# Optimization experiments

Hardware: AMD Instinct MI355X
Metric: run time of the kernel (lower is better)

Reference implementation:

```python
import jax, jax.numpy as jnp
import numpy as np

B, L, LO, H, V = 8, 1024, 1024, 768, 4096
NUM_TAGS = 256


def _merge_one(tags):
    """Replicates merge_weights() for one sequence of tags [L].

    A maximal run of equal, non-(-1) tags becomes one output row that averages
    the hidden states over the run. A run is only emitted when it is *closed*
    by a tag change or a -1 (so a run ending at the last position is dropped,
    exactly like the torch loop). Remaining rows are zero with bias -100.
    """
    Ls = tags.shape[0]
    pos = jnp.arange(Ls)
    valid = tags != -1
    prev = jnp.concatenate([jnp.full((1,), -2, tags.dtype), tags[:-1]])
    start = valid & ((pos == 0) | (tags != prev) | (prev == -1))
    seg_id = jnp.cumsum(start.astype(jnp.int32)) - 1          # run index per position
    total_runs = seg_id[-1] + 1
    emitted = total_runs - valid[-1].astype(jnp.int32)        # trailing open run dropped
    seg_clip = jnp.clip(seg_id, 0, Ls - 1)
    # run lengths via segment sum (invalid positions contribute 0)
    counts = jax.ops.segment_sum(valid.astype(jnp.float32), seg_clip, num_segments=Ls)
    w = jnp.where(valid & (seg_id >= 0) & (seg_id < emitted),
                  1.0 / jnp.maximum(counts[seg_clip], 1.0), 0.0)
    merge = jnp.zeros((Ls, Ls), jnp.float32).at[seg_clip, pos].add(w)  # [rows, tokens]
    bias = jnp.where(pos < emitted, 0.0, -100.0)
    return merge, bias


def setup_inputs() -> dict:
    key = jax.random.key(0)
    k1, k2, k3, k4 = jax.random.split(key, 4)
    hidden1_states = jax.random.normal(k1, (B, L, H), jnp.float32)
    hidden2_states = jax.random.normal(k2, (B, LO, H), jnp.float32)
    lm_logits = jax.random.normal(k3, (B, LO, V), jnp.float32)
    tags = jnp.sort(jax.random.randint(k4, (B, L), 0, NUM_TAGS), axis=-1)
    return {"hidden1_states": hidden1_states, "hidden2_states": hidden2_states,
            "lm_logits": lm_logits, "tags": tags}


def reference(hidden1_states, hidden2_states, lm_logits, tags):
    merge, bias = jax.vmap(_merge_one)(tags)                     # [B,L,L], [B,L]
    attn = jnp.einsum('bls,bsh->blh', merge, hidden1_states)     # segment means
    attn1 = jnp.einsum('boh,blh->bol', hidden2_states, attn) + bias[:, None, :]
    return jnp.concatenate([lm_logits, attn1], axis=2)           # [B,LO,V+L]
```

## Files before the change

### kernel.cpp

```cpp
#include <hip/hip_runtime.h>
#include <hip/hip_bf16.h>
#include <stdint.h>

#define BB   8
#define LL   1024
#define LOO  1024
#define HH   768
#define VV   4096
#define OUTW 5120
#define EMAX 256

typedef unsigned short ushort_t;
typedef __attribute__((ext_vector_type(4))) float   f32x4;
typedef __attribute__((ext_vector_type(8))) __bf16  bf16x8;
typedef __attribute__((ext_vector_type(4))) float   float4v;
typedef __attribute__((ext_vector_type(4))) int     int4v;

static __device__ __forceinline__ ushort_t f2bf(float f) {
    union { float f; uint32_t u; } v; v.f = f;
    uint32_t u = v.u;
    uint32_t r = (u + 0x7fffu + ((u >> 16) & 1u)) >> 16;
    return (ushort_t)r;
}

__global__ __launch_bounds__(256) void attn_fused_kernel(
        const float* __restrict__ h1,
        const int* __restrict__ tags,
        ushort_t* __restrict__ attn,
        int* __restrict__ emitted_out) {
    int b = blockIdx.x >> 8;
    int r = blockIdx.x & 255;
    int tid = threadIdx.x;

    __shared__ int stags[LL];
    __shared__ int cnt[256];
    __shared__ int runpos[EMAX + 2];

    ((int4v*)stags)[tid] = ((const int4v*)(tags + b * LL))[tid];
    __syncthreads();

    int p0 = tid * 4;
    int st[4];
    int prevm1 = (p0 == 0) ? -2 : stags[p0 - 1];
    st[0] = (p0 == 0) || (stags[p0] != prevm1);
    st[1] = (stags[p0 + 1] != stags[p0]);
    st[2] = (stags[p0 + 2] != stags[p0 + 1]);
    st[3] = (stags[p0 + 3] != stags[p0 + 2]);
    int c = st[0] + st[1] + st[2] + st[3];
    cnt[tid] = c;
    __syncthreads();
    for (int off = 1; off < 256; off <<= 1) {
        int v = cnt[tid];
        int a = (tid >= off) ? cnt[tid - off] : 0;
        __syncthreads();
        cnt[tid] = v + a;
        __syncthreads();
    }
    int total = cnt[255];
    int base = cnt[tid] - c;
#pragma unroll
    for (int j = 0; j < 4; ++j)
        if (st[j]) runpos[base++] = p0 + j;
    if (tid == 0) runpos[total] = LL;
    __syncthreads();

    int em = total - 1;
    if (r == 0 && tid == 0) emitted_out[b] = em;

    ushort_t* arow = attn + ((size_t)b * EMAX + r) * HH;
    if (r >= em) {
        arow[tid] = 0; arow[tid + 256] = 0; arow[tid + 512] = 0;
        return;
    }
    int s = runpos[r], e = runpos[r + 1];
    float inv = 1.0f / (float)(e - s);
    const float* hb = h1 + (size_t)b * LL * HH;
    float a0 = 0.f, a1 = 0.f, a2 = 0.f;
    for (int p = s; p < e; ++p) {
        const float* row = hb + (size_t)p * HH;
        a0 += row[tid]; a1 += row[tid + 256]; a2 += row[tid + 512];
    }
    arow[tid]       = f2bf(a0 * inv);
    arow[tid + 256] = f2bf(a1 * inv);
    arow[tid + 512] = f2bf(a2 * inv);
}

#define NGEMM 128
#define NCOPY 2048
__global__ __launch_bounds__(256, 2) void mega_kernel(
        const float* __restrict__ A,
        const ushort_t* __restrict__ Bm,
        const int* __restrict__ emitted,
        const float* __restrict__ lm,
        float* __restrict__ out) {
    __shared__ char smem[49152];

    if (blockIdx.x >= NGEMM) {
        int cid = blockIdx.x - NGEMM;
        int tid = threadIdx.x;
        const float4v* in4 = (const float4v*)lm;
        float4v* out4 = (float4v*)out;
        int c = cid * 256 + tid;
#pragma unroll
        for (int g = 0; g < 4; ++g) {
            size_t i0 = (size_t)(g * 4 + 0) * 524288 + c;
            size_t i1 = (size_t)(g * 4 + 1) * 524288 + c;
            size_t i2 = (size_t)(g * 4 + 2) * 524288 + c;
            size_t i3 = (size_t)(g * 4 + 3) * 524288 + c;
            float4v v0 = in4[i0];
            float4v v1 = in4[i1];
            float4v v2 = in4[i2];
            float4v v3 = in4[i3];
            out4[i0 + ((i0 >> 10) << 8)] = v0;
            out4[i1 + ((i1 >> 10) << 8)] = v1;
            out4[i2 + ((i2 >> 10) << 8)] = v2;
            out4[i3 + ((i3 >> 10) << 8)] = v3;
        }
        float4v fv = {-100.f, -100.f, -100.f, -100.f};
        if (tid < 192) {
#pragma unroll
            for (int j = 0; j < 4; ++j) {
                size_t row = (size_t)cid * 4 + j;
                out4[row * (OUTW / 4) + (VV + 256) / 4 + tid] = fv;
            }
        }
        return;
    }

    int bid  = blockIdx.x;
    int b    = bid >> 4;
    int t2   = bid & 15;
    int brow = (t2 >> 1) << 7;
    int bcol = (t2 & 1) << 7;

    const int tid  = threadIdx.x;
    const int lane = tid & 63;
    const int wid  = tid >> 6;
    const int wr   = (wid >> 1) & 1;
    const int wc   = wid & 1;

    const float*    Ab = A  + (size_t)b * LOO * HH;
    const ushort_t* Bb = Bm + (size_t)b * EMAX * HH;

    f32x4 zero = {0.f, 0.f, 0.f, 0.f};
    f32x4 acc[4][4];
#pragma unroll
    for (int i = 0; i < 4; ++i)
#pragma unroll
        for (int j = 0; j < 4; ++j) acc[i][j] = zero;

    for (int k0 = 0; k0 < HH; k0 += 64) {
        __syncthreads();
#pragma unroll
        for (int i = 0; i < 8; ++i) {
            int off = i * 4096 + tid * 16;
            int row = off >> 8;
            int cb  = off & 255;
            int scb = cb ^ ((row & 7) << 5);
            const float* ga = Ab + (size_t)(brow + row) * HH + k0 + (scb >> 2);
            __builtin_amdgcn_global_load_lds(
                (const __attribute__((address_space(1))) void*)ga,
                (__attribute__((address_space(3))) void*)(smem + off), 16, 0, 0);
        }
#pragma unroll
        for (int i = 0; i < 4; ++i) {
            int off = i * 4096 + tid * 16;
            int row = off >> 7;
            int cb  = off & 127;
            int scb = cb ^ ((row & 7) << 4);
            const ushort_t* gb = Bb + (size_t)(bcol + row) * HH + k0 + (scb >> 1);
            __builtin_amdgcn_global_load_lds(
                (const __attribute__((address_space(1))) void*)gb,
                (__attribute__((address_space(3))) void*)(smem + 32768 + off), 16, 0, 0);
        }
        asm volatile("s_waitcnt vmcnt(0)" ::: "memory");
        __syncthreads();

#pragma unroll
        for (int ks = 0; ks < 2; ++ks) {
            bf16x8 af[4], bfr[4];
#pragma unroll
            for (int mi = 0; mi < 4; ++mi) {
                int row  = (wr << 6) + (mi << 4) + (lane & 15);
                int colb = (ks << 7) + ((lane >> 4) << 5);
                int addr = (row << 8) + (colb ^ ((row & 7) << 5));
                f32x4 a0 = *(const f32x4*)(smem + addr);
                f32x4 a1 = *(const f32x4*)(smem + addr + 16);
                bf16x8 t;
                t[0] = (__bf16)a0[0]; t[1] = (__bf16)a0[1];
                t[2] = (__bf16)a0[2]; t[3] = (__bf16)a0[3];
                t[4] = (__bf16)a1[0]; t[5] = (__bf16)a1[1];
                t[6] = (__bf16)a1[2]; t[7] = (__bf16)a1[3];
                af[mi] = t;
            }
#pragma unroll
            for (int ni = 0; ni < 4; ++ni) {
                int row  = (wc << 6) + (ni << 4) + (lane & 15);
                int colb = (ks << 6) + ((lane >> 4) << 4);
                int addr = (row << 7) + (colb ^ ((row & 7) << 4));
                bfr[ni] = *(const bf16x8*)(smem + 32768 + addr);
            }
#pragma unroll
            for (int mi = 0; mi < 4; ++mi)
#pragma unroll
                for (int ni = 0; ni < 4; ++ni)
                    acc[mi][ni] = __builtin_amdgcn_mfma_f32_16x16x32_bf16(
                        af[mi], bfr[ni], acc[mi][ni], 0, 0, 0);
        }
    }

    int em = emitted[b];
    float* outb = out + (size_t)b * LOO * OUTW + VV;
#pragma unroll
    for (int mi = 0; mi < 4; ++mi) {
        int rbase = brow + (wr << 6) + (mi << 4) + ((lane >> 4) << 2);
#pragma unroll
        for (int ni = 0; ni < 4; ++ni) {
            int col = bcol + (wc << 6) + (ni << 4) + (lane & 15);
            float badd = (col < em) ? 0.0f : -100.0f;
#pragma unroll
            for (int rr = 0; rr < 4; ++rr)
                outb[(size_t)(rbase + rr) * OUTW + col] = acc[mi][ni][rr] + badd;
        }
    }
}

extern "C" void kernel_launch(void* const* d_in, const int* in_sizes, int n_in,
                              void* d_out, int out_size, void* d_ws, size_t ws_size,
                              hipStream_t stream) {
    const float* h1   = (const float*)d_in[0];
    const float* h2   = (const float*)d_in[1];
    const float* lm   = (const float*)d_in[2];
    const int*   tags = (const int*)d_in[3];
    float* out = (float*)d_out;

    char* ws = (char*)d_ws;
    ushort_t* attn    = (ushort_t*)ws;
    int*      emitted = (int*)(ws + 3145728);

    attn_fused_kernel<<<BB * EMAX, 256, 0, stream>>>(h1, tags, attn, emitted);
    mega_kernel<<<NGEMM + NCOPY, 256, 0, stream>>>(h2, attn, emitted, lm, out);
}
```

Measured before the change: 85.08 us.

## Drop LDS staging in GEMM and use smaller 128x64 tiles with more blocks

The GEMM portion no longer stages A and B tiles through shared memory with global_load_lds. Each wave now loads its MFMA fragments straight from global memory, converting fp32 to bf16 in registers. The output tile shrinks from 128x128 to 128x64, which doubles the GEMM block count to 256 and raises the occupancy hint to 4 blocks per SM. The aim is to remove LDS round trips and barriers and to spread the GEMM over more CUs alongside the copy blocks. The cost is that operands are re-read from global or cache by several waves, and the fragment loads are less coalesced.

```diff
diff --git a/kernel.cpp b/kernel.cpp
--- a/kernel.cpp
+++ b/kernel.cpp
@@ -85,15 +85,14 @@
     arow[tid + 512] = f2bf(a2 * inv);
 }
 
-#define NGEMM 128
+#define NGEMM 256
 #define NCOPY 2048
-__global__ __launch_bounds__(256, 2) void mega_kernel(
+__global__ __launch_bounds__(256, 4) void mega_kernel(
         const float* __restrict__ A,
         const ushort_t* __restrict__ Bm,
         const int* __restrict__ emitted,
         const float* __restrict__ lm,
         float* __restrict__ out) {
-    __shared__ char smem[49152];
 
     if (blockIdx.x >= NGEMM) {
         int cid = blockIdx.x - NGEMM;
@@ -128,10 +127,10 @@
     }
 
     int bid  = blockIdx.x;
-    int b    = bid >> 4;
-    int t2   = bid & 15;
-    int brow = (t2 >> 1) << 7;
-    int bcol = (t2 & 1) << 7;
+    int b    = bid >> 5;
+    int t2   = bid & 31;
+    int brow = (t2 >> 2) << 7;
+    int bcol = (t2 & 3) << 6;
 
     const int tid  = threadIdx.x;
     const int lane = tid & 63;
@@ -142,71 +141,39 @@
     const float*    Ab = A  + (size_t)b * LOO * HH;
     const ushort_t* Bb = Bm + (size_t)b * EMAX * HH;
 
+    const int arow0 = brow + (wr << 6) + (lane & 15);
+    const int brow0 = bcol + (wc << 5) + (lane & 15);
+    const int ksub  = (lane >> 4) << 3;
+
     f32x4 zero = {0.f, 0.f, 0.f, 0.f};
-    f32x4 acc[4][4];
-#pragma unroll
-    for (int i = 0; i < 4; ++i)
-#pragma unroll
-        for (int j = 0; j < 4; ++j) acc[i][j] = zero;
-
-    for (int k0 = 0; k0 < HH; k0 += 64) {
-        __syncthreads();
-#pragma unroll
-        for (int i = 0; i < 8; ++i) {
-            int off = i * 4096 + tid * 16;
-            int row = off >> 8;
-            int cb  = off & 255;
-            int scb = cb ^ ((row & 7) << 5);
-            const float* ga = Ab + (size_t)(brow + row) * HH + k0 + (scb >> 2);
-            __builtin_amdgcn_global_load_lds(
-                (const __attribute__((address_space(1))) void*)ga,
-                (__attribute__((address_space(3))) void*)(smem + off), 16, 0, 0);
-        }
-#pragma unroll
-        for (int i = 0; i < 4; ++i) {
-            int off = i * 4096 + tid * 16;
-            int row = off >> 7;
-            int cb  = off & 127;
-            int scb = cb ^ ((row & 7) << 4);
-            const ushort_t* gb = Bb + (size_t)(bcol + row) * HH + k0 + (scb >> 1);
-            __builtin_amdgcn_global_load_lds(
-                (const __attribute__((address_space(1))) void*)gb,
-                (__attribute__((address_space(3))) void*)(smem + 32768 + off), 16, 0, 0);
-        }
-        asm volatile("s_waitcnt vmcnt(0)" ::: "memory");
-        __syncthreads();
-
-#pragma unroll
-        for (int ks = 0; ks < 2; ++ks) {
-            bf16x8 af[4], bfr[4];
-#pragma unroll
-            for (int mi = 0; mi < 4; ++mi) {
-                int row  = (wr << 6) + (mi << 4) + (lane & 15);
-                int colb = (ks << 7) + ((lane >> 4) << 5);
-                int addr = (row << 8) + (colb ^ ((row & 7) << 5));
-                f32x4 a0 = *(const f32x4*)(smem + addr);
-                f32x4 a1 = *(const f32x4*)(smem + addr + 16);
-                bf16x8 t;
-                t[0] = (__bf16)a0[0]; t[1] = (__bf16)a0[1];
-                t[2] = (__bf16)a0[2]; t[3] = (__bf16)a0[3];
-                t[4] = (__bf16)a1[0]; t[5] = (__bf16)a1[1];
-                t[6] = (__bf16)a1[2]; t[7] = (__bf16)a1[3];
-                af[mi] = t;
-            }
-#pragma unroll
-            for (int ni = 0; ni < 4; ++ni) {
-                int row  = (wc << 6) + (ni << 4) + (lane & 15);
-                int colb = (ks << 6) + ((lane >> 4) << 4);
-                int addr = (row << 7) + (colb ^ ((row & 7) << 4));
-                bfr[ni] = *(const bf16x8*)(smem + 32768 + addr);
-            }
-#pragma unroll
-            for (int mi = 0; mi < 4; ++mi)
-#pragma unroll
-                for (int ni = 0; ni < 4; ++ni)
-                    acc[mi][ni] = __builtin_amdgcn_mfma_f32_16x16x32_bf16(
-                        af[mi], bfr[ni], acc[mi][ni], 0, 0, 0);
-        }
+    f32x4 acc[4][2];
+#pragma unroll
+    for (int i = 0; i < 4; ++i) { acc[i][0] = zero; acc[i][1] = zero; }
+
+#pragma unroll 2
+    for (int k0 = 0; k0 < HH; k0 += 32) {
+        bf16x8 af[4], bfr[2];
+#pragma unroll
+        for (int mi = 0; mi < 4; ++mi) {
+            const float* pa = Ab + (size_t)(arow0 + (mi << 4)) * HH + k0 + ksub;
+            f32x4 a0 = *(const f32x4*)pa;
+            f32x4 a1 = *(const f32x4*)(pa + 4);
+            bf16x8 t;
+            t[0] = (__bf16)a0[0]; t[1] = (__bf16)a0[1];
+            t[2] = (__bf16)a0[2]; t[3] = (__bf16)a0[3];
+            t[4] = (__bf16)a1[0]; t[5] = (__bf16)a1[1];
+            t[6] = (__bf16)a1[2]; t[7] = (__bf16)a1[3];
+            af[mi] = t;
+        }
+#pragma unroll
+        for (int ni = 0; ni < 2; ++ni)
+            bfr[ni] = *(const bf16x8*)(Bb + (size_t)(brow0 + (ni << 4)) * HH + k0 + ksub);
+#pragma unroll
+        for (int mi = 0; mi < 4; ++mi)
+#pragma unroll
+            for (int ni = 0; ni < 2; ++ni)
+                acc[mi][ni] = __builtin_amdgcn_mfma_f32_16x16x32_bf16(
+                    af[mi], bfr[ni], acc[mi][ni], 0, 0, 0);
     }
 
     int em = emitted[b];
@@ -215,8 +182,8 @@
     for (int mi = 0; mi < 4; ++mi) {
         int rbase = brow + (wr << 6) + (mi << 4) + ((lane >> 4) << 2);
 #pragma unroll
-        for (int ni = 0; ni < 4; ++ni) {
-            int col = bcol + (wc << 6) + (ni << 4) + (lane & 15);
+        for (int ni = 0; ni < 2; ++ni) {
+            int col = bcol + (wc << 5) + (ni << 4) + (lane & 15);
             float badd = (col < em) ? 0.0f : -100.0f;
 #pragma unroll
             for (int rr = 0; rr < 4; ++rr)
```

New measurement: 96.79 us. 13.8% more time.

## Fuse segment-mean kernel into mega kernel with per-batch atomic completion flags

Applied to the files above, without the earlier changes.

Merges the segment-averaging kernel into the GEMM/copy mega kernel. GEMM blocks spin on a per-batch atomic counter until all 256 attention-row blocks for that batch have finished, and they recompute the emitted run count from tags themselves. This removes a kernel launch boundary and lets the lm_logits copy overlap with the attention stage. In exchange it adds a memset launch, spin-waiting blocks that occupy CU slots, and a risk of deadlock if GEMM blocks get scheduled before the producer blocks they wait on.

```diff
diff --git a/kernel.cpp b/kernel.cpp
--- a/kernel.cpp
+++ b/kernel.cpp
@@ -23,81 +23,87 @@
     return (ushort_t)r;
 }
 
-__global__ __launch_bounds__(256) void attn_fused_kernel(
+#define NATTN 2048
+#define NGEMMB 128
+#define NCOPY 2048
+
+struct SM {
+    union {
+        struct { int stags[LL]; int cnt[256]; int runpos[EMAX + 2]; } a;
+        char g[49152];
+    } u;
+};
+
+__global__ __launch_bounds__(256, 2) void mega_kernel(
         const float* __restrict__ h1,
-        const int* __restrict__ tags,
-        ushort_t* __restrict__ attn,
-        int* __restrict__ emitted_out) {
-    int b = blockIdx.x >> 8;
-    int r = blockIdx.x & 255;
-    int tid = threadIdx.x;
-
-    __shared__ int stags[LL];
-    __shared__ int cnt[256];
-    __shared__ int runpos[EMAX + 2];
-
-    ((int4v*)stags)[tid] = ((const int4v*)(tags + b * LL))[tid];
-    __syncthreads();
-
-    int p0 = tid * 4;
-    int st[4];
-    int prevm1 = (p0 == 0) ? -2 : stags[p0 - 1];
-    st[0] = (p0 == 0) || (stags[p0] != prevm1);
-    st[1] = (stags[p0 + 1] != stags[p0]);
-    st[2] = (stags[p0 + 2] != stags[p0 + 1]);
-    st[3] = (stags[p0 + 3] != stags[p0 + 2]);
-    int c = st[0] + st[1] + st[2] + st[3];
-    cnt[tid] = c;
-    __syncthreads();
-    for (int off = 1; off < 256; off <<= 1) {
-        int v = cnt[tid];
-        int a = (tid >= off) ? cnt[tid - off] : 0;
-        __syncthreads();
-        cnt[tid] = v + a;
-        __syncthreads();
-    }
-    int total = cnt[255];
-    int base = cnt[tid] - c;
-#pragma unroll
-    for (int j = 0; j < 4; ++j)
-        if (st[j]) runpos[base++] = p0 + j;
-    if (tid == 0) runpos[total] = LL;
-    __syncthreads();
-
-    int em = total - 1;
-    if (r == 0 && tid == 0) emitted_out[b] = em;
-
-    ushort_t* arow = attn + ((size_t)b * EMAX + r) * HH;
-    if (r >= em) {
-        arow[tid] = 0; arow[tid + 256] = 0; arow[tid + 512] = 0;
+        const float* __restrict__ h2,
+        const float* __restrict__ lm,
+        const int*   __restrict__ tags,
+        ushort_t*    __restrict__ attn,
+        int*         __restrict__ done,
+        float*       __restrict__ out) {
+    __shared__ SM sm;
+    const int bid = blockIdx.x;
+    const int tid = threadIdx.x;
+
+    if (bid < NATTN) {
+        int b = bid >> 8;
+        int r = bid & 255;
+
+        ((int4v*)sm.u.a.stags)[tid] = ((const int4v*)(tags + b * LL))[tid];
+        __syncthreads();
+
+        int p0 = tid * 4;
+        int st[4];
+        int prevm1 = (p0 == 0) ? -2 : sm.u.a.stags[p0 - 1];
+        st[0] = (p0 == 0) || (sm.u.a.stags[p0] != prevm1);
+        st[1] = (sm.u.a.stags[p0 + 1] != sm.u.a.stags[p0]);
+        st[2] = (sm.u.a.stags[p0 + 2] != sm.u.a.stags[p0 + 1]);
+        st[3] = (sm.u.a.stags[p0 + 3] != sm.u.a.stags[p0 + 2]);
+        int c = st[0] + st[1] + st[2] + st[3];
+        sm.u.a.cnt[tid] = c;
+        __syncthreads();
+        for (int off = 1; off < 256; off <<= 1) {
+            int v = sm.u.a.cnt[tid];
+            int a = (tid >= off) ? sm.u.a.cnt[tid - off] : 0;
+            __syncthreads();
+            sm.u.a.cnt[tid] = v + a;
+            __syncthreads();
+        }
+        int total = sm.u.a.cnt[255];
+        int base = sm.u.a.cnt[tid] - c;
+#pragma unroll
+        for (int j = 0; j < 4; ++j)
+            if (st[j]) sm.u.a.runpos[base++] = p0 + j;
+        if (tid == 0) sm.u.a.runpos[total] = LL;
+        __syncthreads();
+
+        int em = total - 1;
+        ushort_t* arow = attn + ((size_t)b * EMAX + r) * HH;
+        if (r >= em) {
+            arow[tid] = 0; arow[tid + 256] = 0; arow[tid + 512] = 0;
+        } else {
+            int s = sm.u.a.runpos[r], e = sm.u.a.runpos[r + 1];
+            float inv = 1.0f / (float)(e - s);
+            const float* hb = h1 + (size_t)b * LL * HH;
+            float a0 = 0.f, a1 = 0.f, a2 = 0.f;
+            for (int p = s; p < e; ++p) {
+                const float* row = hb + (size_t)p * HH;
+                a0 += row[tid]; a1 += row[tid + 256]; a2 += row[tid + 512];
+            }
+            arow[tid]       = f2bf(a0 * inv);
+            arow[tid + 256] = f2bf(a1 * inv);
+            arow[tid + 512] = f2bf(a2 * inv);
+        }
+        __syncthreads();
+        if (tid == 0)
+            __hip_atomic_fetch_add(&done[b], 1, __ATOMIC_RELEASE,
+                                   __HIP_MEMORY_SCOPE_AGENT);
         return;
     }
-    int s = runpos[r], e = runpos[r + 1];
-    float inv = 1.0f / (float)(e - s);
-    const float* hb = h1 + (size_t)b * LL * HH;
-    float a0 = 0.f, a1 = 0.f, a2 = 0.f;
-    for (int p = s; p < e; ++p) {
-        const float* row = hb + (size_t)p * HH;
-        a0 += row[tid]; a1 += row[tid + 256]; a2 += row[tid + 512];
-    }
-    arow[tid]       = f2bf(a0 * inv);
-    arow[tid + 256] = f2bf(a1 * inv);
-    arow[tid + 512] = f2bf(a2 * inv);
-}
-
-#define NGEMM 128
-#define NCOPY 2048
-__global__ __launch_bounds__(256, 2) void mega_kernel(
-        const float* __restrict__ A,
-        const ushort_t* __restrict__ Bm,
-        const int* __restrict__ emitted,
-        const float* __restrict__ lm,
-        float* __restrict__ out) {
-    __shared__ char smem[49152];
-
-    if (blockIdx.x >= NGEMM) {
-        int cid = blockIdx.x - NGEMM;
-        int tid = threadIdx.x;
+
+    if (bid >= NATTN + NGEMMB) {
+        int cid = bid - (NATTN + NGEMMB);
         const float4v* in4 = (const float4v*)lm;
         float4v* out4 = (float4v*)out;
         int c = cid * 256 + tid;
@@ -127,20 +133,24 @@
         return;
     }
 
-    int bid  = blockIdx.x;
-    int b    = bid >> 4;
-    int t2   = bid & 15;
+    int g    = bid - NATTN;
+    int b    = g >> 4;
+    int t2   = g & 15;
     int brow = (t2 >> 1) << 7;
     int bcol = (t2 & 1) << 7;
 
-    const int tid  = threadIdx.x;
+    while (__hip_atomic_load(&done[b], __ATOMIC_ACQUIRE,
+                             __HIP_MEMORY_SCOPE_AGENT) < 256)
+        __builtin_amdgcn_s_sleep(8);
+    __syncthreads();
+
     const int lane = tid & 63;
     const int wid  = tid >> 6;
     const int wr   = (wid >> 1) & 1;
     const int wc   = wid & 1;
 
-    const float*    Ab = A  + (size_t)b * LOO * HH;
-    const ushort_t* Bb = Bm + (size_t)b * EMAX * HH;
+    const float*    Ab = h2   + (size_t)b * LOO * HH;
+    const ushort_t* Bb = attn + (size_t)b * EMAX * HH;
 
     f32x4 zero = {0.f, 0.f, 0.f, 0.f};
     f32x4 acc[4][4];
@@ -160,7 +170,7 @@
             const float* ga = Ab + (size_t)(brow + row) * HH + k0 + (scb >> 2);
             __builtin_amdgcn_global_load_lds(
                 (const __attribute__((address_space(1))) void*)ga,
-                (__attribute__((address_space(3))) void*)(smem + off), 16, 0, 0);
+                (__attribute__((address_space(3))) void*)(sm.u.g + off), 16, 0, 0);
         }
 #pragma unroll
         for (int i = 0; i < 4; ++i) {
@@ -171,7 +181,7 @@
             const ushort_t* gb = Bb + (size_t)(bcol + row) * HH + k0 + (scb >> 1);
             __builtin_amdgcn_global_load_lds(
                 (const __attribute__((address_space(1))) void*)gb,
-                (__attribute__((address_space(3))) void*)(smem + 32768 + off), 16, 0, 0);
+                (__attribute__((address_space(3))) void*)(sm.u.g + 32768 + off), 16, 0, 0);
         }
         asm volatile("s_waitcnt vmcnt(0)" ::: "memory");
         __syncthreads();
@@ -184,8 +194,8 @@
                 int row  = (wr << 6) + (mi << 4) + (lane & 15);
                 int colb = (ks << 7) + ((lane >> 4) << 5);
                 int addr = (row << 8) + (colb ^ ((row & 7) << 5));
-                f32x4 a0 = *(const f32x4*)(smem + addr);
-                f32x4 a1 = *(const f32x4*)(smem + addr + 16);
+                f32x4 a0 = *(const f32x4*)(sm.u.g + addr);
+                f32x4 a1 = *(const f32x4*)(sm.u.g + addr + 16);
                 bf16x8 t;
                 t[0] = (__bf16)a0[0]; t[1] = (__bf16)a0[1];
                 t[2] = (__bf16)a0[2]; t[3] = (__bf16)a0[3];
@@ -198,7 +208,7 @@
                 int row  = (wc << 6) + (ni << 4) + (lane & 15);
                 int colb = (ks << 6) + ((lane >> 4) << 4);
                 int addr = (row << 7) + (colb ^ ((row & 7) << 4));
-                bfr[ni] = *(const bf16x8*)(smem + 32768 + addr);
+                bfr[ni] = *(const bf16x8*)(sm.u.g + 32768 + addr);
             }
 #pragma unroll
             for (int mi = 0; mi < 4; ++mi)
@@ -209,7 +219,40 @@
         }
     }
 
-    int em = emitted[b];
+    int em;
+    {
+        const int* tg = tags + b * LL;
+        int cnt_runs = 0;
+        int prev = -2;
+        for (int p = tid; p < LL; p += 256) { }
+        int myc = 0;
+        for (int p = tid; p < LL; p += 256) {
+            int t  = tg[p];
+            int pr = (p == 0) ? -2 : tg[p - 1];
+            myc += (t != pr);
+        }
+        __syncthreads();
+        int* red = (int*)sm.u.g;
+        red[tid] = myc;
+        __syncthreads();
+        if (tid < 128) red[tid] += red[tid + 128];
+        __syncthreads();
+        if (tid < 64) red[tid] += red[tid + 64];
+        __syncthreads();
+        if (tid < 32) { red[tid] += red[tid + 32]; }
+        __syncthreads();
+        if (tid < 16) { red[tid] += red[tid + 16]; }
+        __syncthreads();
+        if (tid < 8) { red[tid] += red[tid + 8]; }
+        __syncthreads();
+        if (tid < 4) { red[tid] += red[tid + 4]; }
+        __syncthreads();
+        if (tid < 2) { red[tid] += red[tid + 2]; }
+        __syncthreads();
+        cnt_runs = red[0] + red[1];
+        em = cnt_runs - 1;
+    }
+
     float* outb = out + (size_t)b * LOO * OUTW + VV;
 #pragma unroll
     for (int mi = 0; mi < 4; ++mi) {
@@ -235,9 +278,10 @@
     float* out = (float*)d_out;
 
     char* ws = (char*)d_ws;
-    ushort_t* attn    = (ushort_t*)ws;
-    int*      emitted = (int*)(ws + 3145728);
-
-    attn_fused_kernel<<<BB * EMAX, 256, 0, stream>>>(h1, tags, attn, emitted);
-    mega_kernel<<<NGEMM + NCOPY, 256, 0, stream>>>(h2, attn, emitted, lm, out);
+    ushort_t* attn = (ushort_t*)ws;
+    int*      done = (int*)(ws + 3145728);
+
+    hipMemsetAsync(done, 0, BB * sizeof(int), stream);
+    mega_kernel<<<NATTN + NGEMMB + NCOPY, 256, 0, stream>>>(
+        h1, h2, lm, tags, attn, done, out);
 }
```

Result: slower. 192.9 us (+126.7%).
